# Optimization experiments

Hardware: AMD Instinct MI355X
Metric: run time of the kernel (lower is better)

The kernel has to match this reference:

```python
import jax, jax.numpy as jnp
import numpy as np


def setup_inputs() -> dict:
    key = jax.random.key(0)
    k1, k2, k3, k4 = jax.random.split(key, 4)
    T, B, I, H = 512, 64, 1024, 1024
    sigma = 0.01
    return {
        "inputs": jax.random.normal(k1, (T, B, I), dtype=jnp.float32),
        "W_xh": jax.random.normal(k2, (I, H), dtype=jnp.float32) * sigma,
        "W_hh": jax.random.normal(k3, (H, H), dtype=jnp.float32) * sigma,
        "b_h": jnp.zeros((H,), dtype=jnp.float32),
    }


def reference(inputs, W_xh, W_hh, b_h):
    # Tanh RNN: h_t = tanh(x_t @ W_xh + h_{t-1} @ W_hh + b_h), h_{-1} = 0.
    # (state=None in the torch module contributes 0 on the first step,
    #  identical to an all-zeros initial state.)
    B, H = inputs.shape[1], W_hh.shape[0]
    # Precompute the input projections for all timesteps in one big GEMM.
    xW = jnp.einsum("tbi,ih->tbh", inputs, W_xh) + b_h  # [T, B, H]

    def step(h, xw_t):
        h = jnp.tanh(xw_t + h @ W_hh)
        return h, h

    h0 = jnp.zeros((B, H), dtype=inputs.dtype)
    last_state, outputs = jax.lax.scan(step, h0, xW)
    return outputs, last_state
```

## Files before the change

kernel.cpp:

```cpp
#include <hip/hip_runtime.h>
#include <hip/hip_bf16.h>
#include <stdint.h>

typedef __attribute__((ext_vector_type(8))) short short8;
typedef __attribute__((ext_vector_type(4))) short short4v;
typedef __attribute__((ext_vector_type(4))) float f32x4;
typedef __attribute__((ext_vector_type(4))) int int4v;

#define T_STEPS 512
#define BATCH 64
#define HDIM 1024
#define MROWS (T_STEPS * BATCH)

__device__ __forceinline__ unsigned short f2bf(float f) {
  unsigned int u = __float_as_uint(f);
  u += 0x7FFFu + ((u >> 16) & 1u);
  return (unsigned short)(u >> 16);
}

__global__ __launch_bounds__(256) void transpose_cvt(const float* __restrict__ src,
                                                     unsigned short* __restrict__ dst) {
  __shared__ unsigned short tile[32][36];
  int b = blockIdx.x;
  int tr = b >> 5, tc = b & 31;
  int t = threadIdx.x;
  int i = t >> 3, j4 = (t & 7) << 2;
  const float4 v = *(const float4*)(src + (size_t)(tr * 32 + i) * 1024 + tc * 32 + j4);
  tile[i][j4 + 0] = f2bf(v.x);
  tile[i][j4 + 1] = f2bf(v.y);
  tile[i][j4 + 2] = f2bf(v.z);
  tile[i][j4 + 3] = f2bf(v.w);
  __syncthreads();
  int c = t >> 3, r4 = (t & 7) << 2;
  short4v o;
  o[0] = (short)tile[r4 + 0][c];
  o[1] = (short)tile[r4 + 1][c];
  o[2] = (short)tile[r4 + 2][c];
  o[3] = (short)tile[r4 + 3][c];
  *(short4v*)(dst + (size_t)(tc * 32 + c) * 1024 + tr * 32 + r4) = o;
}

__global__ __launch_bounds__(256, 2) void xw_gemm(const float* __restrict__ A,
                                                  const unsigned short* __restrict__ BT,
                                                  const float* __restrict__ bias,
                                                  float* __restrict__ C) {
  __shared__ unsigned short As[128][40];
  __shared__ unsigned short Bs[128][40];
  int b = blockIdx.x;
  int swz = (b & 7) * 256 + (b >> 3);
  int tn = swz & 7, tm = swz >> 3;
  int t = threadIdx.x, lane = t & 63, wave = t >> 6;
  int l15 = lane & 15, l4 = lane >> 4;
  int wm = wave >> 1, wn = wave & 1;

  f32x4 acc[4][4];
#pragma unroll
  for (int i = 0; i < 4; ++i)
#pragma unroll
    for (int j = 0; j < 4; ++j) acc[i][j] = (f32x4){0.f, 0.f, 0.f, 0.f};

  int sm = t >> 1, sh = (t & 1) << 4;
  const float* a_src = A + (size_t)(tm * 128 + sm) * 1024 + sh;
  const unsigned short* b_src = BT + (size_t)(tn * 128 + sm) * 1024 + sh;

  for (int kt = 0; kt < 32; ++kt) {
    float4 av0 = *(const float4*)(a_src + kt * 32 + 0);
    float4 av1 = *(const float4*)(a_src + kt * 32 + 4);
    float4 av2 = *(const float4*)(a_src + kt * 32 + 8);
    float4 av3 = *(const float4*)(a_src + kt * 32 + 12);
    short8 w0, w1;
    w0[0] = (short)f2bf(av0.x); w0[1] = (short)f2bf(av0.y);
    w0[2] = (short)f2bf(av0.z); w0[3] = (short)f2bf(av0.w);
    w0[4] = (short)f2bf(av1.x); w0[5] = (short)f2bf(av1.y);
    w0[6] = (short)f2bf(av1.z); w0[7] = (short)f2bf(av1.w);
    w1[0] = (short)f2bf(av2.x); w1[1] = (short)f2bf(av2.y);
    w1[2] = (short)f2bf(av2.z); w1[3] = (short)f2bf(av2.w);
    w1[4] = (short)f2bf(av3.x); w1[5] = (short)f2bf(av3.y);
    w1[6] = (short)f2bf(av3.z); w1[7] = (short)f2bf(av3.w);
    *(short8*)&As[sm][sh] = w0;
    *(short8*)&As[sm][sh + 8] = w1;
    short8 bv0 = *(const short8*)(b_src + kt * 32 + 0);
    short8 bv1 = *(const short8*)(b_src + kt * 32 + 8);
    *(short8*)&Bs[sm][sh] = bv0;
    *(short8*)&Bs[sm][sh + 8] = bv1;
    __syncthreads();

    short8 af[4], bfr[4];
#pragma unroll
    for (int i = 0; i < 4; ++i) af[i] = *(const short8*)&As[wm * 64 + i * 16 + l15][8 * l4];
#pragma unroll
    for (int j = 0; j < 4; ++j) bfr[j] = *(const short8*)&Bs[wn * 64 + j * 16 + l15][8 * l4];
#pragma unroll
    for (int i = 0; i < 4; ++i)
#pragma unroll
      for (int j = 0; j < 4; ++j)
        acc[i][j] = __builtin_amdgcn_mfma_f32_16x16x32_bf16(af[i], bfr[j], acc[i][j], 0, 0, 0);
    __syncthreads();
  }

#pragma unroll
  for (int i = 0; i < 4; ++i) {
    int row0 = tm * 128 + wm * 64 + i * 16 + l4 * 4;
#pragma unroll
    for (int j = 0; j < 4; ++j) {
      int col = tn * 128 + wn * 64 + j * 16 + l15;
      float bv = bias[col];
#pragma unroll
      for (int r = 0; r < 4; ++r)
        C[(size_t)(row0 + r) * 1024 + col] = acc[i][j][r] + bv;
    }
  }
}

__device__ __forceinline__ void coh_store_dword(int* p, int v) {
  asm volatile("global_store_dword %0, %1, off sc0 sc1" ::"v"(p), "v"(v) : "memory");
}
__device__ __forceinline__ void coh_load_dwordx4_issue(int4v* dst, const int* p) {
  asm volatile("global_load_dwordx4 %0, %1, off sc0 sc1" : "=&v"(*dst) : "v"(p) : "memory");
}

__global__ __launch_bounds__(256, 1) void rnn_scan(const unsigned short* __restrict__ whhT,
                                                   float* __restrict__ out,
                                                   int* __restrict__ hbuf) {
  int wg = blockIdx.x;
  int xcd = wg & 7;
  int bg = xcd >> 1;
  int cg = ((wg >> 3) << 1) | (xcd & 1);
  int t = threadIdx.x, lane = t & 63, wave = t >> 6;
  int l15 = lane & 15, l4 = lane >> 4;

  __shared__ __align__(16) float red[4][64][4];

  short8 bfrag[8];
#pragma unroll
  for (int i = 0; i < 8; ++i)
    bfrag[i] = *(const short8*)(whhT + (size_t)(cg * 16 + l15) * 1024 + wave * 256 + i * 32 + 8 * l4);

  int row = bg * 16 + l4 * 4 + wave;
  int col = cg * 16 + l15;
  const int* cons_base0 = hbuf + (size_t)(bg * 16 + l15) * 1024 + wave * 256 + 8 * l4;
  int* prod_base = hbuf + (size_t)row * 1024 + col;

  for (int s = 0; s < T_STEPS; ++s) {
    size_t oidx = ((size_t)s * BATCH + row) * HDIM + col;
    float xw = out[oidx];

    f32x4 acc = (f32x4){0.f, 0.f, 0.f, 0.f};
    if (s > 0) {
      const int* cb = cons_base0 + (size_t)((s - 1) & 1) * BATCH * HDIM;
      unsigned int tagv = (unsigned int)s;
      int4v q[16];
      for (;;) {
#pragma unroll
        for (int i = 0; i < 8; ++i) {
          coh_load_dwordx4_issue(&q[2 * i], cb + i * 32);
          coh_load_dwordx4_issue(&q[2 * i + 1], cb + i * 32 + 4);
        }
        asm volatile("s_waitcnt vmcnt(0)" ::: "memory");
        __builtin_amdgcn_sched_barrier(0);
        unsigned int bad = 0;
#pragma unroll
        for (int i = 0; i < 16; ++i) {
          bad |= ((unsigned int)q[i][0] >> 16) ^ tagv;
          bad |= ((unsigned int)q[i][1] >> 16) ^ tagv;
          bad |= ((unsigned int)q[i][2] >> 16) ^ tagv;
          bad |= ((unsigned int)q[i][3] >> 16) ^ tagv;
        }
        if (__all(bad == 0)) break;
        __builtin_amdgcn_s_sleep(1);
      }
#pragma unroll
      for (int i = 0; i < 8; ++i) {
        int4v lo = q[2 * i], hi = q[2 * i + 1];
        int4v pk;
        pk[0] = (lo[0] & 0xffff) | (lo[1] << 16);
        pk[1] = (lo[2] & 0xffff) | (lo[3] << 16);
        pk[2] = (hi[0] & 0xffff) | (hi[1] << 16);
        pk[3] = (hi[2] & 0xffff) | (hi[3] << 16);
        acc = __builtin_amdgcn_mfma_f32_16x16x32_bf16(*(short8*)&pk, bfrag[i], acc, 0, 0, 0);
      }
    }
    *(f32x4*)&red[wave][lane][0] = acc;
    __syncthreads();
    float sum = red[0][lane][wave] + red[1][lane][wave] + red[2][lane][wave] + red[3][lane][wave];
    float hv = tanhf(xw + sum);
    out[oidx] = hv;
    coh_store_dword(prod_base + (size_t)(s & 1) * BATCH * HDIM,
                    (int)(((unsigned int)(s + 1) << 16) | (unsigned int)f2bf(hv)));
    if (s == T_STEPS - 1)
      out[(size_t)MROWS * HDIM + (size_t)row * HDIM + col] = hv;
    __syncthreads();
  }
}

extern "C" void kernel_launch(void* const* d_in, const int* in_sizes, int n_in,
                              void* d_out, int out_size, void* d_ws, size_t ws_size,
                              hipStream_t stream) {
  const float* inp = (const float*)d_in[0];
  const float* wxh = (const float*)d_in[1];
  const float* whh = (const float*)d_in[2];
  const float* bh  = (const float*)d_in[3];
  float* out = (float*)d_out;

  char* ws = (char*)d_ws;
  unsigned short* whhT = (unsigned short*)(ws);
  unsigned short* wxhT = (unsigned short*)(ws + (2u << 20));
  int* hbuf = (int*)(ws + (4u << 20));

  hipMemsetAsync(hbuf, 0, 2u * BATCH * HDIM * sizeof(int), stream);
  transpose_cvt<<<1024, 256, 0, stream>>>(whh, whhT);
  transpose_cvt<<<1024, 256, 0, stream>>>(wxh, wxhT);
  xw_gemm<<<2048, 256, 0, stream>>>(inp, wxhT, bh, out);
  rnn_scan<<<256, 256, 0, stream>>>(whhT, out, hbuf);
}
```

Measured before the change: 2.978 ms.

## Shrink scan grid to 64 workgroups with 64-column tiles and sentinel polling

The recurrent scan now uses 64 workgroups instead of 256. Each workgroup owns a 16-row by 64-column tile and keeps four column slices of W_hh in registers, so one loaded h fragment feeds four MFMAs. Polling first spins on a single sentinel dwordx4 load before issuing the full fragment load, which cuts coherent-load traffic while waiting. A double-buffered reduction array removes the second barrier per step. The trade-off is fewer CUs doing the per-step work and higher register pressure (32 short8 weight fragments), in exchange for fewer producers and consumers in the cross-workgroup synchronization.

After: 2.667 ms. -10.4%, faster.

```diff
diff --git a/kernel.cpp b/kernel.cpp
--- a/kernel.cpp
+++ b/kernel.cpp
@@ -123,73 +123,111 @@
                                                    float* __restrict__ out,
                                                    int* __restrict__ hbuf) {
   int wg = blockIdx.x;
-  int xcd = wg & 7;
-  int bg = xcd >> 1;
-  int cg = ((wg >> 3) << 1) | (xcd & 1);
+  int bg = wg >> 4;
+  int cg = wg & 15;
   int t = threadIdx.x, lane = t & 63, wave = t >> 6;
   int l15 = lane & 15, l4 = lane >> 4;
 
-  __shared__ __align__(16) float red[4][64][4];
-
-  short8 bfrag[8];
-#pragma unroll
-  for (int i = 0; i < 8; ++i)
-    bfrag[i] = *(const short8*)(whhT + (size_t)(cg * 16 + l15) * 1024 + wave * 256 + i * 32 + 8 * l4);
-
-  int row = bg * 16 + l4 * 4 + wave;
-  int col = cg * 16 + l15;
-  const int* cons_base0 = hbuf + (size_t)(bg * 16 + l15) * 1024 + wave * 256 + 8 * l4;
-  int* prod_base = hbuf + (size_t)row * 1024 + col;
+  __shared__ __align__(16) float red[2][4][64][4][4];
+
+  short8 wfrag[4][8];
+#pragma unroll
+  for (int c = 0; c < 4; ++c)
+#pragma unroll
+    for (int m = 0; m < 8; ++m)
+      wfrag[c][m] = *(const short8*)(whhT + (size_t)(64 * cg + 16 * c + l15) * 1024 +
+                                     256 * wave + 32 * m + 8 * l4);
+
+  int colw = 64 * cg + 16 * wave + l15;
 
   for (int s = 0; s < T_STEPS; ++s) {
-    size_t oidx = ((size_t)s * BATCH + row) * HDIM + col;
-    float xw = out[oidx];
-
-    f32x4 acc = (f32x4){0.f, 0.f, 0.f, 0.f};
+    float xw[4];
+#pragma unroll
+    for (int r = 0; r < 4; ++r)
+      xw[r] = out[((size_t)s * BATCH + bg * 16 + l4 * 4 + r) * HDIM + colw];
+
+    f32x4 acc[4];
+#pragma unroll
+    for (int c = 0; c < 4; ++c) acc[c] = (f32x4){0.f, 0.f, 0.f, 0.f};
+
     if (s > 0) {
-      const int* cb = cons_base0 + (size_t)((s - 1) & 1) * BATCH * HDIM;
-      unsigned int tagv = (unsigned int)s;
+      const unsigned tagv = (unsigned)s;
+      const int* base = hbuf + (((s - 1) & 1) << 16) + (16 * bg + l15) * 1024 + 256 * wave;
+      const int* sp = base + 64 * l4 + 4 * l15;
       int4v q[16];
       for (;;) {
-#pragma unroll
-        for (int i = 0; i < 8; ++i) {
-          coh_load_dwordx4_issue(&q[2 * i], cb + i * 32);
-          coh_load_dwordx4_issue(&q[2 * i + 1], cb + i * 32 + 4);
+        for (;;) {
+          int4v sv;
+          coh_load_dwordx4_issue(&sv, sp);
+          asm volatile("s_waitcnt vmcnt(0)" ::: "memory");
+          unsigned bad = (((unsigned)sv[0] >> 16) ^ tagv) | (((unsigned)sv[1] >> 16) ^ tagv) |
+                         (((unsigned)sv[2] >> 16) ^ tagv) | (((unsigned)sv[3] >> 16) ^ tagv);
+          if (__all(bad == 0)) break;
+          __builtin_amdgcn_s_sleep(2);
+        }
+#pragma unroll
+        for (int jj = 0; jj < 4; ++jj) {
+          const int* fb = base + 64 * jj + 8 * l4;
+          coh_load_dwordx4_issue(&q[jj * 4 + 0], fb);
+          coh_load_dwordx4_issue(&q[jj * 4 + 1], fb + 4);
+          coh_load_dwordx4_issue(&q[jj * 4 + 2], fb + 32);
+          coh_load_dwordx4_issue(&q[jj * 4 + 3], fb + 36);
         }
         asm volatile("s_waitcnt vmcnt(0)" ::: "memory");
         __builtin_amdgcn_sched_barrier(0);
-        unsigned int bad = 0;
+        unsigned bad = 0;
 #pragma unroll
         for (int i = 0; i < 16; ++i) {
-          bad |= ((unsigned int)q[i][0] >> 16) ^ tagv;
-          bad |= ((unsigned int)q[i][1] >> 16) ^ tagv;
-          bad |= ((unsigned int)q[i][2] >> 16) ^ tagv;
-          bad |= ((unsigned int)q[i][3] >> 16) ^ tagv;
+          bad |= (((unsigned)q[i][0] >> 16) ^ tagv) | (((unsigned)q[i][1] >> 16) ^ tagv) |
+                 (((unsigned)q[i][2] >> 16) ^ tagv) | (((unsigned)q[i][3] >> 16) ^ tagv);
         }
         if (__all(bad == 0)) break;
         __builtin_amdgcn_s_sleep(1);
       }
 #pragma unroll
-      for (int i = 0; i < 8; ++i) {
-        int4v lo = q[2 * i], hi = q[2 * i + 1];
-        int4v pk;
-        pk[0] = (lo[0] & 0xffff) | (lo[1] << 16);
-        pk[1] = (lo[2] & 0xffff) | (lo[3] << 16);
-        pk[2] = (hi[0] & 0xffff) | (hi[1] << 16);
-        pk[3] = (hi[2] & 0xffff) | (hi[3] << 16);
-        acc = __builtin_amdgcn_mfma_f32_16x16x32_bf16(*(short8*)&pk, bfrag[i], acc, 0, 0, 0);
+      for (int jj = 0; jj < 4; ++jj) {
+        int4v a0 = q[jj * 4 + 0], a1 = q[jj * 4 + 1], a2 = q[jj * 4 + 2], a3 = q[jj * 4 + 3];
+        int4v p0, p1;
+        p0[0] = (a0[0] & 0xffff) | (a0[1] << 16);
+        p0[1] = (a0[2] & 0xffff) | (a0[3] << 16);
+        p0[2] = (a1[0] & 0xffff) | (a1[1] << 16);
+        p0[3] = (a1[2] & 0xffff) | (a1[3] << 16);
+        p1[0] = (a2[0] & 0xffff) | (a2[1] << 16);
+        p1[1] = (a2[2] & 0xffff) | (a2[3] << 16);
+        p1[2] = (a3[0] & 0xffff) | (a3[1] << 16);
+        p1[3] = (a3[2] & 0xffff) | (a3[3] << 16);
+#pragma unroll
+        for (int c = 0; c < 4; ++c) {
+          acc[c] = __builtin_amdgcn_mfma_f32_16x16x32_bf16(*(short8*)&p0, wfrag[c][2 * jj],
+                                                           acc[c], 0, 0, 0);
+          acc[c] = __builtin_amdgcn_mfma_f32_16x16x32_bf16(*(short8*)&p1, wfrag[c][2 * jj + 1],
+                                                           acc[c], 0, 0, 0);
+        }
       }
     }
-    *(f32x4*)&red[wave][lane][0] = acc;
+
+    int p = s & 1;
+#pragma unroll
+    for (int c = 0; c < 4; ++c) *(f32x4*)&red[p][wave][lane][c][0] = acc[c];
     __syncthreads();
-    float sum = red[0][lane][wave] + red[1][lane][wave] + red[2][lane][wave] + red[3][lane][wave];
-    float hv = tanhf(xw + sum);
-    out[oidx] = hv;
-    coh_store_dword(prod_base + (size_t)(s & 1) * BATCH * HDIM,
-                    (int)(((unsigned int)(s + 1) << 16) | (unsigned int)f2bf(hv)));
-    if (s == T_STEPS - 1)
-      out[(size_t)MROWS * HDIM + (size_t)row * HDIM + col] = hv;
-    __syncthreads();
+    f32x4 hsum;
+#pragma unroll
+    for (int r = 0; r < 4; ++r)
+      hsum[r] = red[p][0][lane][wave][r] + red[p][1][lane][wave][r] +
+                red[p][2][lane][wave][r] + red[p][3][lane][wave][r];
+
+#pragma unroll
+    for (int r = 0; r < 4; ++r) {
+      int row = bg * 16 + l4 * 4 + r;
+      size_t oidx = ((size_t)s * BATCH + row) * HDIM + colw;
+      float hv = tanhf(xw[r] + hsum[r]);
+      out[oidx] = hv;
+      if (s != T_STEPS - 1)
+        coh_store_dword(hbuf + ((s & 1) << 16) + row * 1024 + colw,
+                        (int)(((unsigned)(s + 1) << 16) | (unsigned)f2bf(hv)));
+      else
+        out[(size_t)MROWS * HDIM + (size_t)row * HDIM + colw] = hv;
+    }
   }
 }
 
@@ -211,5 +249,5 @@
   transpose_cvt<<<1024, 256, 0, stream>>>(whh, whhT);
   transpose_cvt<<<1024, 256, 0, stream>>>(wxh, wxhT);
   xw_gemm<<<2048, 256, 0, stream>>>(inp, wxhT, bh, out);
-  rnn_scan<<<256, 256, 0, stream>>>(whhT, out, hbuf);
-}
+  rnn_scan<<<64, 256, 0, stream>>>(whhT, out, hbuf);
+}
```
